# Kernel optimization log

Hardware: AMD Instinct MI355X
Metric: run time of the kernel (lower is better)

Reference implementation:

```python
import jax, jax.numpy as jnp
import numpy as np
from jax import lax

K = 3  # kernel_size
DN = ('NCHW', 'OIHW', 'NCHW')


def _conv(x, w, b, pad):
    out = lax.conv_general_dilated(x, w, window_strides=(1, 1),
                                   padding=((pad, pad), (pad, pad)),
                                   dimension_numbers=DN)
    return out + b[None, :, None, None]


def setup_inputs() -> dict:
    key = jax.random.key(0)
    ks = jax.random.split(key, 6)
    N, C, H, W = 8, 64, 128, 128
    x = jax.random.normal(ks[0], (N, C, H, W), dtype=jnp.float32)
    y = jax.random.normal(ks[1], (N, C, H, W), dtype=jnp.float32)
    w1 = jax.random.normal(ks[2], (C, C, 3, 3), dtype=jnp.float32) * 0.05
    b1 = jax.random.normal(ks[3], (C,), dtype=jnp.float32) * 0.05
    w2 = jax.random.normal(ks[4], (C * K * K, C, 1, 1), dtype=jnp.float32) * 0.05
    b2 = jax.random.normal(ks[5], (C * K * K,), dtype=jnp.float32) * 0.05
    return {"x": x, "y": y, "w1": w1, "b1": b1, "w2": w2, "b2": b2}


def reference(x, y, w1, b1, w2, b2):
    N, C, H, W = x.shape
    # kernel generation: 3x3 conv (C->C) then 1x1 conv (C -> C*9)
    h = _conv(y, w1, b1, pad=1)
    kernel = _conv(h, w2, b2, pad=0).reshape(N, C, K * K, H, W)
    # unfold x (3x3, pad 1): patch ordering (kh, kw) row-major per channel,
    # matching nn.Unfold's (C, kh, kw) channel layout after the reshape.
    xp = jnp.pad(x, ((0, 0), (0, 0), (1, 1), (1, 1)))
    patches = jnp.stack([xp[:, :, i:i + H, j:j + W]
                         for i in range(K) for j in range(K)], axis=2)
    # per-pixel dynamic conv: elementwise multiply + reduce over the 9 taps
    return (patches * kernel).sum(axis=2)
```

## Files before the change

kernel.cpp:

```cpp
#include <hip/hip_runtime.h>

#define C   64
#define H   128
#define W   128
#define HW  (H * W)
#define NB  8

using bf16x8 = __attribute__((ext_vector_type(8))) short;
using f32x4  = __attribute__((ext_vector_type(4))) float;

__device__ __forceinline__ unsigned short f2bf(float f) {
    unsigned u = __float_as_uint(f);
    return (unsigned short)((u + 0x7fffu + ((u >> 16) & 1u)) >> 16);
}

__global__ __launch_bounds__(256) void prep_weights(
    const float* __restrict__ w1, const float* __restrict__ w2,
    const float* __restrict__ b2,
    unsigned short* __restrict__ w1f, unsigned short* __restrict__ w2f,
    float* __restrict__ b2f)
{
    int i = blockIdx.x * 256 + threadIdx.x;
    if (i < 36864) {
        {
            int j = i & 7, lane = (i >> 3) & 63, m = (i >> 9) & 3, s = i >> 11;
            int l15 = lane & 15, lhi = lane >> 4;
            int co = m * 16 + l15;
            int kk = s * 32 + lhi * 8 + j;
            int tap = kk >> 6, k = kk & 63;
            w1f[i] = f2bf(w1[co * 576 + k * 9 + tap]);
        }
        {
            int j = i & 7, lane = (i >> 3) & 63, ks = (i >> 9) & 1, t9 = i >> 10;
            int tap = t9 % 9, cc = t9 / 9;
            int cp = cc * 16 + (lane & 15);
            int k = ks * 32 + (lane >> 4) * 8 + j;
            w2f[i] = f2bf(w2[(cp * 9 + tap) * 64 + k]);
        }
    }
    if (i < 9216) {
        int r = i & 3, lane = (i >> 2) & 63, t9 = i >> 8;
        int tap = t9 % 9, cc = t9 / 9;
        int cpp = cc * 16 + ((lane >> 4) << 2) + r;
        b2f[i] = b2[cpp * 9 + tap];
    }
}

__global__ __launch_bounds__(256) void transpose_y(
    const float* __restrict__ y, unsigned short* __restrict__ yT)
{
    __shared__ unsigned short tl[64 * 64];
    const int t = threadIdx.x, b = blockIdx.x;
    const int n = b & 7, tile = b >> 3;
    const int px0 = tile * 64;
    const int wv = t >> 6, l = t & 63;

    const float* src = y + (size_t)n * C * HW + px0 + l;
    #pragma unroll
    for (int i = 0; i < 8; ++i) {
        int ch = wv * 16 + i * 2;
        float v0 = src[(size_t)ch * HW];
        float v1 = src[(size_t)(ch + 1) * HW];
        unsigned pk = (unsigned)f2bf(v0) | ((unsigned)f2bf(v1) << 16);
        *(unsigned*)&tl[l * 64 + (ch ^ ((l & 7) << 3))] = pk;
    }
    __syncthreads();

    const int px = t >> 2, c0 = (t & 3) * 16;
    const int xr = (px & 7) << 3;
    uint4 w0 = *(const uint4*)&tl[px * 64 + (c0 ^ xr)];
    uint4 w1 = *(const uint4*)&tl[px * 64 + ((c0 + 8) ^ xr)];
    unsigned short* dst = yT + ((size_t)n * HW + px0 + px) * 64 + c0;
    *(uint4*)&dst[0] = w0;
    *(uint4*)&dst[8] = w1;
}

__global__ __launch_bounds__(256, 1) void fused_dc(
    const float* __restrict__ x,
    const unsigned short* __restrict__ yT,
    const unsigned short* __restrict__ w1f,
    const float* __restrict__ b1,
    const unsigned short* __restrict__ w2f,
    const float* __restrict__ b2f,
    float* __restrict__ out)
{
    __shared__ unsigned short h_lds[128 * 64];
    __shared__ __align__(16) unsigned short w_lds[18432];

    const int t = threadIdx.x, b = blockIdx.x;
    const int n = b & 7;
    const int p = b >> 3;
    const int wid = t >> 6, lane = t & 63;
    const int l15 = lane & 15, lhi = lane >> 4;
    const int qw = wid << 5;

    const unsigned short* yTn = yT + (size_t)n * HW * 64;

    f32x4 acc[4][2];
    #pragma unroll
    for (int m = 0; m < 4; ++m)
        #pragma unroll
        for (int pt = 0; pt < 2; ++pt)
            acc[m][pt] = f32x4{0.f, 0.f, 0.f, 0.f};

    #pragma unroll
    for (int half = 0; half < 2; ++half) {
        if (half) __syncthreads();
        {
            const uint4* src = (const uint4*)w1f + half * 2304;
            uint4* dst = (uint4*)w_lds;
            #pragma unroll
            for (int j = 0; j < 9; ++j) dst[t + 256 * j] = src[t + 256 * j];
        }
        __syncthreads();

        #pragma unroll
        for (int sp = 0; sp < 9; ++sp) {
            const int s = half * 9 + sp;
            const int tap = s >> 1, trow = tap / 3, dq = tap % 3 - 1;
            const int k0 = (s & 1) * 32 + lhi * 8;
            const int grow = p + trow - 1;
            const bool rok = (unsigned)grow < (unsigned)H;
            const int cg = rok ? grow : 0;

            bf16x8 Y[2];
            #pragma unroll
            for (int pt = 0; pt < 2; ++pt) {
                int col = qw + pt * 16 + l15 + dq;
                bool ok = rok && ((unsigned)col < (unsigned)W);
                int cl = col < 0 ? 0 : (col > 127 ? 127 : col);
                bf16x8 v = *(const bf16x8*)&yTn[((size_t)cg * W + cl) * 64 + k0];
                Y[pt] = ok ? v : (bf16x8)0;
            }
            bf16x8 Wf[4];
            #pragma unroll
            for (int m = 0; m < 4; ++m)
                Wf[m] = *(const bf16x8*)&w_lds[((sp * 4 + m) * 64 + lane) * 8];

            #pragma unroll
            for (int m = 0; m < 4; ++m)
                #pragma unroll
                for (int pt = 0; pt < 2; ++pt)
                    acc[m][pt] = __builtin_amdgcn_mfma_f32_16x16x32_bf16(
                        Wf[m], Y[pt], acc[m][pt], 0, 0, 0);
        }
    }

    #pragma unroll
    for (int m = 0; m < 4; ++m) {
        float4 bq1 = *(const float4*)&b1[m * 16 + lhi * 4];
        #pragma unroll
        for (int pt = 0; pt < 2; ++pt) {
            int px = qw + pt * 16 + l15;
            int cb = m * 16 + lhi * 4;
            unsigned lo = (unsigned)f2bf(acc[m][pt][0] + bq1.x)
                        | ((unsigned)f2bf(acc[m][pt][1] + bq1.y) << 16);
            unsigned hi = (unsigned)f2bf(acc[m][pt][2] + bq1.z)
                        | ((unsigned)f2bf(acc[m][pt][3] + bq1.w) << 16);
            uint2 pk; pk.x = lo; pk.y = hi;
            *(uint2*)&h_lds[px * 64 + (cb ^ ((px & 7) << 3))] = pk;
        }
    }

    bf16x8 hA[2][2];
    #pragma unroll
    for (int pt = 0; pt < 2; ++pt)
        #pragma unroll
        for (int ks = 0; ks < 2; ++ks) {
            int px = qw + pt * 16 + l15;
            int ko = ks * 32 + lhi * 8;
            hA[pt][ks] = *(const bf16x8*)&h_lds[px * 64 + (ko ^ ((px & 7) << 3))];
        }

    const float* xn_ = x + (size_t)n * C * HW;
    float* out_ = out + (size_t)n * C * HW;

    #pragma unroll
    for (int cc = 0; cc < 4; ++cc) {
        __syncthreads();
        {
            const uint4* src = (const uint4*)(w2f + cc * 9216);
            uint4* dst = (uint4*)w_lds;
            #pragma unroll
            for (int j = 0; j < 4; ++j) dst[t + 256 * j] = src[t + 256 * j];
            if (t < 128) dst[t + 1024] = src[t + 1024];
            const uint4* srcb = (const uint4*)(b2f + cc * 2304);
            uint4* dstb = (uint4*)(w_lds + 9216);
            #pragma unroll
            for (int j = 0; j < 2; ++j) dstb[t + 256 * j] = srcb[t + 256 * j];
            if (t < 64) dstb[t + 512] = srcb[t + 512];
        }
        __syncthreads();

        const float* b2l = (const float*)(w_lds + 9216);

        bf16x8 wA0[2], wA1[2];
        f32x4  bq[2];
        float  xv[2][2][4];

        auto loadTap = [&](int tap, int bi) {
            wA0[bi] = *(const bf16x8*)&w_lds[((tap * 2 + 0) * 64 + lane) * 8];
            wA1[bi] = *(const bf16x8*)&w_lds[((tap * 2 + 1) * 64 + lane) * 8];
            bq[bi]  = *(const f32x4*)&b2l[(tap * 64 + lane) * 4];
            const int ri = tap / 3, cj = tap % 3;
            const int grow = p + ri - 1;
            const bool rok = (unsigned)grow < (unsigned)H;
            const int cr = rok ? grow : 0;
            #pragma unroll
            for (int pt = 0; pt < 2; ++pt) {
                int col = qw + pt * 16 + l15 + cj - 1;
                bool ok = rok && ((unsigned)col < (unsigned)W);
                int cl = col < 0 ? 0 : (col > 127 ? 127 : col);
                const float* xb = xn_ + (size_t)(cc * 16 + lhi * 4) * HW
                                + (size_t)cr * W + cl;
                #pragma unroll
                for (int r = 0; r < 4; ++r) {
                    float v = xb[(size_t)r * HW];
                    xv[bi][pt][r] = ok ? v : 0.f;
                }
            }
        };

        f32x4 oacc[2];
        oacc[0] = f32x4{0.f, 0.f, 0.f, 0.f};
        oacc[1] = f32x4{0.f, 0.f, 0.f, 0.f};

        loadTap(0, 0);
        #pragma unroll
        for (int tap = 0; tap < 9; ++tap) {
            if (tap < 8) loadTap(tap + 1, (tap + 1) & 1);
            const int bi = tap & 1;
            #pragma unroll
            for (int pt = 0; pt < 2; ++pt) {
                f32x4 kf = __builtin_amdgcn_mfma_f32_16x16x32_bf16(
                    wA0[bi], hA[pt][0], bq[bi], 0, 0, 0);
                kf = __builtin_amdgcn_mfma_f32_16x16x32_bf16(
                    wA1[bi], hA[pt][1], kf, 0, 0, 0);
                #pragma unroll
                for (int r = 0; r < 4; ++r)
                    oacc[pt][r] = fmaf(kf[r], xv[bi][pt][r], oacc[pt][r]);
            }
        }

        #pragma unroll
        for (int pt = 0; pt < 2; ++pt)
            #pragma unroll
            for (int r = 0; r < 4; ++r)
                out_[(size_t)(cc * 16 + lhi * 4 + r) * HW
                     + (size_t)p * W + qw + pt * 16 + l15] = oacc[pt][r];
    }
}

extern "C" void kernel_launch(void* const* d_in, const int* in_sizes, int n_in,
                              void* d_out, int out_size, void* d_ws, size_t ws_size,
                              hipStream_t stream)
{
    const float* x  = (const float*)d_in[0];
    const float* y  = (const float*)d_in[1];
    const float* w1 = (const float*)d_in[2];
    const float* b1 = (const float*)d_in[3];
    const float* w2 = (const float*)d_in[4];
    const float* b2 = (const float*)d_in[5];
    float* out = (float*)d_out;

    char* ws = (char*)d_ws;
    unsigned short* yT  = (unsigned short*)ws;
    unsigned short* w1f = (unsigned short*)(ws + 16777216);
    unsigned short* w2f = (unsigned short*)(ws + 16777216 + 73728);
    float*          b2f = (float*)(ws + 16777216 + 147456);

    prep_weights<<<144, 256, 0, stream>>>(w1, w2, b2, w1f, w2f, b2f);
    transpose_y<<<NB * HW / 64, 256, 0, stream>>>(y, yT);
    fused_dc<<<NB * H, 256, 0, stream>>>(x, yT, w1f, b1, w2f, b2f, out);
}
```

Before: 67.16 us.

## Double-buffer weight staging with async global-to-LDS loads

Replaces the synchronous copy of weights into shared memory with direct global-to-LDS asynchronous loads into two alternating buffers. The next weight chunk is staged while the current one feeds MFMA work, across both the 3x3 conv phase (six chunks) and the 1x1 kernel-gen phase. The second-stage bias is now read straight from global memory instead of LDS. The intent is to hide weight-load latency behind compute. In exchange there are more barriers, and it relies on the LDS ordering of the async load matching the old layout and on the barriers being enough to see the async writes.

```diff
diff --git a/kernel.cpp b/kernel.cpp
--- a/kernel.cpp
+++ b/kernel.cpp
@@ -12,6 +12,13 @@
 __device__ __forceinline__ unsigned short f2bf(float f) {
     unsigned u = __float_as_uint(f);
     return (unsigned short)((u + 0x7fffu + ((u >> 16) & 1u)) >> 16);
+}
+
+__device__ __forceinline__ void gl_lds16(const void* g, void* l) {
+    __builtin_amdgcn_global_load_lds(
+        (const __attribute__((address_space(1))) unsigned int*)g,
+        (__attribute__((address_space(3))) unsigned int*)l,
+        16, 0, 0);
 }
 
 __global__ __launch_bounds__(256) void prep_weights(
@@ -85,7 +92,7 @@
     float* __restrict__ out)
 {
     __shared__ unsigned short h_lds[128 * 64];
-    __shared__ __align__(16) unsigned short w_lds[18432];
+    __shared__ __align__(16) unsigned short w_lds[2][9216];
 
     const int t = threadIdx.x, b = blockIdx.x;
     const int n = b & 7;
@@ -96,6 +103,25 @@
 
     const unsigned short* yTn = yT + (size_t)n * HW * 64;
 
+    auto stage_p1 = [&](int q, int buf) {
+        const char* src = (const char*)w1f + q * 12288 + t * 16;
+        char* dstb = (char*)&w_lds[buf][0] + wid * 1024;
+        #pragma unroll
+        for (int j = 0; j < 3; ++j)
+            gl_lds16(src + j * 4096, dstb + j * 4096);
+    };
+    auto stage_p2 = [&](int cc, int buf) {
+        const char* src = (const char*)w2f + cc * 18432 + t * 16;
+        char* dstb = (char*)&w_lds[buf][0] + wid * 1024;
+        #pragma unroll
+        for (int j = 0; j < 4; ++j)
+            gl_lds16(src + j * 4096, dstb + j * 4096);
+        if (wid < 2)
+            gl_lds16(src + 4 * 4096, dstb + 4 * 4096);
+    };
+
+    stage_p1(0, 0);
+
     f32x4 acc[4][2];
     #pragma unroll
     for (int m = 0; m < 4; ++m)
@@ -103,20 +129,17 @@
         for (int pt = 0; pt < 2; ++pt)
             acc[m][pt] = f32x4{0.f, 0.f, 0.f, 0.f};
 
-    #pragma unroll
-    for (int half = 0; half < 2; ++half) {
-        if (half) __syncthreads();
-        {
-            const uint4* src = (const uint4*)w1f + half * 2304;
-            uint4* dst = (uint4*)w_lds;
-            #pragma unroll
-            for (int j = 0; j < 9; ++j) dst[t + 256 * j] = src[t + 256 * j];
-        }
-        __syncthreads();
-
-        #pragma unroll
-        for (int sp = 0; sp < 9; ++sp) {
-            const int s = half * 9 + sp;
+    __syncthreads();
+
+    #pragma unroll
+    for (int q = 0; q < 6; ++q) {
+        if (q < 5) stage_p1(q + 1, (q + 1) & 1);
+        else       stage_p2(0, 0);
+
+        const unsigned short* wb = &w_lds[q & 1][0];
+        #pragma unroll
+        for (int sp = 0; sp < 3; ++sp) {
+            const int s = q * 3 + sp;
             const int tap = s >> 1, trow = tap / 3, dq = tap % 3 - 1;
             const int k0 = (s & 1) * 32 + lhi * 8;
             const int grow = p + trow - 1;
@@ -135,7 +158,7 @@
             bf16x8 Wf[4];
             #pragma unroll
             for (int m = 0; m < 4; ++m)
-                Wf[m] = *(const bf16x8*)&w_lds[((sp * 4 + m) * 64 + lane) * 8];
+                Wf[m] = *(const bf16x8*)&wb[((sp * 4 + m) * 64 + lane) * 8];
 
             #pragma unroll
             for (int m = 0; m < 4; ++m)
@@ -144,6 +167,7 @@
                     acc[m][pt] = __builtin_amdgcn_mfma_f32_16x16x32_bf16(
                         Wf[m], Y[pt], acc[m][pt], 0, 0, 0);
         }
+        __syncthreads();
     }
 
     #pragma unroll
@@ -177,31 +201,19 @@
 
     #pragma unroll
     for (int cc = 0; cc < 4; ++cc) {
-        __syncthreads();
-        {
-            const uint4* src = (const uint4*)(w2f + cc * 9216);
-            uint4* dst = (uint4*)w_lds;
-            #pragma unroll
-            for (int j = 0; j < 4; ++j) dst[t + 256 * j] = src[t + 256 * j];
-            if (t < 128) dst[t + 1024] = src[t + 1024];
-            const uint4* srcb = (const uint4*)(b2f + cc * 2304);
-            uint4* dstb = (uint4*)(w_lds + 9216);
-            #pragma unroll
-            for (int j = 0; j < 2; ++j) dstb[t + 256 * j] = srcb[t + 256 * j];
-            if (t < 64) dstb[t + 512] = srcb[t + 512];
-        }
-        __syncthreads();
-
-        const float* b2l = (const float*)(w_lds + 9216);
+        if (cc == 0) __syncthreads();
+        if (cc < 3) stage_p2(cc + 1, (cc + 1) & 1);
+
+        const unsigned short* wb = &w_lds[cc & 1][0];
 
         bf16x8 wA0[2], wA1[2];
         f32x4  bq[2];
         float  xv[2][2][4];
 
         auto loadTap = [&](int tap, int bi) {
-            wA0[bi] = *(const bf16x8*)&w_lds[((tap * 2 + 0) * 64 + lane) * 8];
-            wA1[bi] = *(const bf16x8*)&w_lds[((tap * 2 + 1) * 64 + lane) * 8];
-            bq[bi]  = *(const f32x4*)&b2l[(tap * 64 + lane) * 4];
+            wA0[bi] = *(const bf16x8*)&wb[((tap * 2 + 0) * 64 + lane) * 8];
+            wA1[bi] = *(const bf16x8*)&wb[((tap * 2 + 1) * 64 + lane) * 8];
+            bq[bi]  = *(const f32x4*)&b2f[(size_t)((cc * 9 + tap) * 64 + lane) * 4];
             const int ri = tap / 3, cj = tap % 3;
             const int grow = p + ri - 1;
             const bool rok = (unsigned)grow < (unsigned)H;
@@ -248,6 +260,8 @@
             for (int r = 0; r < 4; ++r)
                 out_[(size_t)(cc * 16 + lhi * 4 + r) * HW
                      + (size_t)p * W + qw + pt * 16 + l15] = oacc[pt][r];
+
+        if (cc < 3) __syncthreads();
     }
 }
 
```

Measured after the change: 66.57 us. About the same (-0.9%).
